# Performance work log

Measured on AMD Instinct MI355X. Metric: run time of the kernel, lower is better.

Reference implementation:

```python
import jax, jax.numpy as jnp
import numpy as np

EPS_LN = 1e-5
EPS_SUM = 1e-5


def setup_inputs() -> dict:
    key = jax.random.key(0)
    ks = jax.random.split(key, 6)
    B, T, F, D = 8, 1024, 512, 64
    x = jax.random.normal(ks[0], (B, T, F), dtype=jnp.float32)
    state = jnp.zeros((B, 1, D * D), dtype=jnp.float32)
    s = 1.0 / np.sqrt(F)
    Wk = jax.random.uniform(ks[1], (F, D), jnp.float32, -s, s)
    Wq = jax.random.uniform(ks[2], (F, D), jnp.float32, -s, s)
    Wv = jax.random.uniform(ks[3], (F, D), jnp.float32, -s, s)
    gamma = jnp.ones((F,), jnp.float32)
    beta = jnp.zeros((F,), jnp.float32)
    return {"x": x, "state": state, "Wk": Wk, "Wq": Wq, "Wv": Wv,
            "gamma": gamma, "beta": beta}


def _layernorm(x, gamma, beta):
    mu = jnp.mean(x, axis=-1, keepdims=True)
    var = jnp.mean(jnp.square(x - mu), axis=-1, keepdims=True)
    return (x - mu) * jax.lax.rsqrt(var + EPS_LN) * gamma + beta


def reference(x, state, Wk, Wq, Wv, gamma, beta):
    B, T, F = x.shape
    D = Wk.shape[1]
    xn = _layernorm(x, gamma, beta)
    K = jax.nn.relu(xn @ Wk)            # [B,T,D]
    Q = jax.nn.relu(xn @ Wq)
    V = xn @ Wv
    # sum normalization (paper)
    K = K / (EPS_SUM + jnp.sum(K, axis=-1, keepdims=True))
    Q = Q / (EPS_SUM + jnp.sum(Q, axis=-1, keepdims=True))
    # outer-product fast weights per step: kv[b,t,i,j] = V[b,t,i] * K[b,t,j]
    kv = jnp.einsum('bti,btj->btij', V, K)        # [B,T,D,D]
    # 'sum' aggregator: running (cumulative) sum seeded by the initial state
    state_seq = state.reshape(B, 1, D, D) + jnp.cumsum(kv, axis=1)  # [B,T,D,D]
    y = jnp.einsum('btij,bti->btj', state_seq, Q)  # [B,T,D]
    return (y, state_seq)
```

## Files before the change

### kernel.cpp

```cpp
#include <hip/hip_runtime.h>

#define BB 8
#define TT 1024
#define FF 512
#define DD 64
#define LCH 16
#define CCH (TT / LCH)
#define PR 8

__device__ __forceinline__ float wave_sum64(float v) {
  #pragma unroll
  for (int m = 32; m >= 1; m >>= 1) v += __shfl_xor(v, m, 64);
  return v;
}

__global__ __launch_bounds__(256, 4) void lnproj_k(
    const float* __restrict__ x,
    const float* __restrict__ gamma, const float* __restrict__ beta,
    const float* __restrict__ Wk, const float* __restrict__ Wq,
    const float* __restrict__ Wv,
    float* __restrict__ Ko, float* __restrict__ Qo, float* __restrict__ Vo) {
  __shared__ float lx[PR * FF];
  __shared__ float part[4 * PR * 3 * DD];
  const int tid = threadIdx.x;
  const int wv = tid >> 6, lane = tid & 63;
  const size_t row0 = (size_t)blockIdx.x * PR;

  {
    const float4* xg = (const float4*)(x + row0 * FF);
    float4* lx4 = (float4*)lx;
    #pragma unroll
    for (int i = 0; i < (PR * FF / 4) / 256; ++i)
      lx4[tid + 256 * i] = xg[tid + 256 * i];
  }
  __syncthreads();

  {
    float g[FF / 64], bt[FF / 64];
    #pragma unroll
    for (int k = 0; k < FF / 64; ++k) {
      g[k]  = gamma[lane + 64 * k];
      bt[k] = beta[lane + 64 * k];
    }
    #pragma unroll
    for (int rr = 0; rr < PR / 4; ++rr) {
      int r = wv * (PR / 4) + rr;
      float v[FF / 64];
      float s = 0.f, ss = 0.f;
      #pragma unroll
      for (int k = 0; k < FF / 64; ++k) {
        v[k] = lx[r * FF + lane + 64 * k];
        s += v[k]; ss += v[k] * v[k];
      }
      s = wave_sum64(s); ss = wave_sum64(ss);
      float m = s * (1.f / FF);
      float var = ss * (1.f / FF) - m * m;
      float rs = rsqrtf(var + 1e-5f);
      #pragma unroll
      for (int k = 0; k < FF / 64; ++k)
        lx[r * FF + lane + 64 * k] = (v[k] - m) * rs * g[k] + bt[k];
    }
  }
  __syncthreads();

  float acc[PR][3];
  #pragma unroll
  for (int r = 0; r < PR; ++r)
    #pragma unroll
    for (int p = 0; p < 3; ++p) acc[r][p] = 0.f;

  const int fbase = wv * (FF / 4);
  #pragma unroll 2
  for (int f0 = fbase; f0 < fbase + FF / 4; f0 += 4) {
    float wk0 = Wk[(f0 + 0) * DD + lane], wk1 = Wk[(f0 + 1) * DD + lane];
    float wk2 = Wk[(f0 + 2) * DD + lane], wk3 = Wk[(f0 + 3) * DD + lane];
    float wq0 = Wq[(f0 + 0) * DD + lane], wq1 = Wq[(f0 + 1) * DD + lane];
    float wq2 = Wq[(f0 + 2) * DD + lane], wq3 = Wq[(f0 + 3) * DD + lane];
    float wv0 = Wv[(f0 + 0) * DD + lane], wv1 = Wv[(f0 + 1) * DD + lane];
    float wv2 = Wv[(f0 + 2) * DD + lane], wv3 = Wv[(f0 + 3) * DD + lane];
    #pragma unroll
    for (int r = 0; r < PR; ++r) {
      float4 xv = *(const float4*)&lx[r * FF + f0];
      acc[r][0] += (xv.x * wk0 + xv.y * wk1) + (xv.z * wk2 + xv.w * wk3);
      acc[r][1] += (xv.x * wq0 + xv.y * wq1) + (xv.z * wq2 + xv.w * wq3);
      acc[r][2] += (xv.x * wv0 + xv.y * wv1) + (xv.z * wv2 + xv.w * wv3);
    }
  }

  #pragma unroll
  for (int r = 0; r < PR; ++r)
    #pragma unroll
    for (int p = 0; p < 3; ++p)
      part[((wv * PR + r) * 3 + p) * DD + lane] = acc[r][p];
  __syncthreads();

  #pragma unroll
  for (int i = 0; i < (PR * 3) / 4; ++i) {
    int pid = wv * ((PR * 3) / 4) + i;
    int r = pid / 3, p = pid - r * 3;
    float val = part[((0 * PR + r) * 3 + p) * DD + lane]
              + part[((1 * PR + r) * 3 + p) * DD + lane]
              + part[((2 * PR + r) * 3 + p) * DD + lane]
              + part[((3 * PR + r) * 3 + p) * DD + lane];
    float* outp = (p == 0) ? Ko : (p == 1) ? Qo : Vo;
    if (p < 2) {
      val = fmaxf(val, 0.f);
      float sm = wave_sum64(val);
      val = val / (1e-5f + sm);
    }
    outp[(row0 + r) * DD + lane] = val;
  }
}

__global__ __launch_bounds__(256) void chunksum_k(const float* __restrict__ Kx,
                                                  const float* __restrict__ Vx,
                                                  float* __restrict__ S) {
  int bc = blockIdx.x, tid = threadIdx.x;
  __shared__ float lk[LCH * DD], lv[LCH * DD];
  for (int e = tid; e < LCH * DD; e += 256) {
    lk[e] = Kx[(size_t)bc * LCH * DD + e];
    lv[e] = Vx[(size_t)bc * LCH * DD + e];
  }
  __syncthreads();
  int j = tid & 63, i0 = (tid >> 6) << 4;
  float acc[16];
  #pragma unroll
  for (int ii = 0; ii < 16; ++ii) acc[ii] = 0.f;
  for (int t = 0; t < LCH; ++t) {
    float kj = lk[t * DD + j];
    #pragma unroll
    for (int ii = 0; ii < 16; ++ii) acc[ii] += lv[t * DD + i0 + ii] * kj;
  }
  float* Sp = S + (size_t)bc * (DD * DD);
  #pragma unroll
  for (int ii = 0; ii < 16; ++ii) Sp[(i0 + ii) * DD + j] = acc[ii];
}

__global__ __launch_bounds__(256) void prefix_k(const float* __restrict__ S,
                                                const float* __restrict__ st0,
                                                float* __restrict__ P) {
  int b = blockIdx.x >> 4;
  int e = ((blockIdx.x & 15) << 8) + threadIdx.x;
  float run = st0[(size_t)b * (DD * DD) + e];
  const float* Sb = S + ((size_t)b * CCH) * (DD * DD) + e;
  float* Pb = P + ((size_t)b * CCH) * (DD * DD) + e;
  for (int c = 0; c < CCH; ++c) {
    Pb[(size_t)c * (DD * DD)] = run;
    run += Sb[(size_t)c * (DD * DD)];
  }
}

__global__ __launch_bounds__(256) void scan_k(const float* __restrict__ Kx,
                     const float* __restrict__ Qx, const float* __restrict__ Vx,
                     const float* __restrict__ P,
                     float* __restrict__ y, float* __restrict__ sout) {
  int bc = blockIdx.x, tid = threadIdx.x;
  int wv = tid >> 6, j = tid & 63;
  int i0 = wv * 16;
  __shared__ float yp[4][LCH][DD];
  float S[16];
  const float* Pp = P + (size_t)bc * (DD * DD);
  #pragma unroll
  for (int ii = 0; ii < 16; ++ii) S[ii] = Pp[(i0 + ii) * DD + j];
  const float* Kb = Kx + (size_t)bc * LCH * DD;
  const float* Vb = Vx + (size_t)bc * LCH * DD;
  const float* Qb = Qx + (size_t)bc * LCH * DD;
  float kreg[LCH];
  #pragma unroll
  for (int t = 0; t < LCH; ++t) kreg[t] = Kb[t * DD + j];
  float* so = sout + (size_t)bc * LCH * (DD * DD) + (size_t)i0 * DD + j;
  for (int t = 0; t < LCH; ++t) {
    const float* Vt = Vb + t * DD + i0;
    const float* Qt = Qb + t * DD + i0;
    float kj = kreg[t];
    float y0 = 0.f, y1 = 0.f, y2 = 0.f, y3 = 0.f;
    float* sot = so + (size_t)t * (DD * DD);
    #pragma unroll
    for (int ii = 0; ii < 16; ii += 4) {
      S[ii]     += Vt[ii]     * kj; sot[(ii)     * DD] = S[ii];     y0 += S[ii]     * Qt[ii];
      S[ii + 1] += Vt[ii + 1] * kj; sot[(ii + 1) * DD] = S[ii + 1]; y1 += S[ii + 1] * Qt[ii + 1];
      S[ii + 2] += Vt[ii + 2] * kj; sot[(ii + 2) * DD] = S[ii + 2]; y2 += S[ii + 2] * Qt[ii + 2];
      S[ii + 3] += Vt[ii + 3] * kj; sot[(ii + 3) * DD] = S[ii + 3]; y3 += S[ii + 3] * Qt[ii + 3];
    }
    yp[wv][t][j] = (y0 + y1) + (y2 + y3);
  }
  __syncthreads();
  float* yo = y + (size_t)bc * LCH * DD;
  #pragma unroll
  for (int tt = 0; tt < LCH / 4; ++tt) {
    int t = wv * (LCH / 4) + tt;
    yo[t * DD + j] = (yp[0][t][j] + yp[1][t][j]) + (yp[2][t][j] + yp[3][t][j]);
  }
}

extern "C" void kernel_launch(void* const* d_in, const int* in_sizes, int n_in,
                              void* d_out, int out_size, void* d_ws, size_t ws_size,
                              hipStream_t stream) {
  const float* x     = (const float*)d_in[0];
  const float* st0   = (const float*)d_in[1];
  const float* Wk    = (const float*)d_in[2];
  const float* Wq    = (const float*)d_in[3];
  const float* Wv    = (const float*)d_in[4];
  const float* gamma = (const float*)d_in[5];
  const float* beta  = (const float*)d_in[6];

  float* out  = (float*)d_out;
  float* yout = out;
  float* sseq = out + (size_t)BB * TT * DD;

  float* ws = (float*)d_ws;
  float* Ko = ws;
  float* Qo = Ko + (size_t)BB * TT * DD;
  float* Vo = Qo + (size_t)BB * TT * DD;
  float* S  = Vo + (size_t)BB * TT * DD;
  float* P  = S  + (size_t)BB * CCH * DD * DD;

  lnproj_k  <<<BB * TT / PR, 256, 0, stream>>>(x, gamma, beta, Wk, Wq, Wv, Ko, Qo, Vo);
  chunksum_k<<<BB * CCH, 256, 0, stream>>>(Ko, Vo, S);
  prefix_k  <<<BB * 16, 256, 0, stream>>>(S, st0, P);
  scan_k    <<<BB * CCH, 256, 0, stream>>>(Ko, Qo, Vo, P, yout, sseq);
}
```

Baseline: 210.3 us.

## Split chunk prefix into parallel segment-sum and segmented-scan kernels

Replaces the serial per-batch prefix over all chunks with a two-pass scheme: first sum chunk states within segments of 8, then each segment scans locally, seeded by the sum of earlier segments. This raises the block count eightfold to expose more parallelism and memory-level concurrency instead of a long dependent loop. It costs an extra kernel launch, an extra read of the chunk-state buffer and a small workspace for segment sums.

```diff
diff --git a/kernel.cpp b/kernel.cpp
--- a/kernel.cpp
+++ b/kernel.cpp
@@ -7,6 +7,8 @@
 #define LCH 16
 #define CCH (TT / LCH)
 #define PR 8
+#define SEG 8
+#define NSEG (CCH / SEG)
 
 __device__ __forceinline__ float wave_sum64(float v) {
   #pragma unroll
@@ -136,17 +138,46 @@
   for (int ii = 0; ii < 16; ++ii) Sp[(i0 + ii) * DD + j] = acc[ii];
 }
 
-__global__ __launch_bounds__(256) void prefix_k(const float* __restrict__ S,
-                                                const float* __restrict__ st0,
-                                                float* __restrict__ P) {
-  int b = blockIdx.x >> 4;
-  int e = ((blockIdx.x & 15) << 8) + threadIdx.x;
+__global__ __launch_bounds__(256) void segsum_k(const float* __restrict__ S,
+                                                float* __restrict__ Z) {
+  int blk = blockIdx.x;
+  int b = blk >> 7;
+  int seg = (blk >> 4) & 7;
+  int e = ((blk & 15) << 8) + threadIdx.x;
+  const float* Sb = S + ((size_t)(b * CCH + seg * SEG)) * (DD * DD) + e;
+  float sv[SEG];
+  #pragma unroll
+  for (int c = 0; c < SEG; ++c) sv[c] = Sb[(size_t)c * (DD * DD)];
+  float acc = 0.f;
+  #pragma unroll
+  for (int c = 0; c < SEG; ++c) acc += sv[c];
+  Z[((size_t)(b * NSEG + seg)) * (DD * DD) + e] = acc;
+}
+
+__global__ __launch_bounds__(256) void segscan_k(const float* __restrict__ S,
+                                                 const float* __restrict__ Z,
+                                                 const float* __restrict__ st0,
+                                                 float* __restrict__ P) {
+  int blk = blockIdx.x;
+  int b = blk >> 7;
+  int seg = (blk >> 4) & 7;
+  int e = ((blk & 15) << 8) + threadIdx.x;
   float run = st0[(size_t)b * (DD * DD) + e];
-  const float* Sb = S + ((size_t)b * CCH) * (DD * DD) + e;
-  float* Pb = P + ((size_t)b * CCH) * (DD * DD) + e;
-  for (int c = 0; c < CCH; ++c) {
+  const float* Zb = Z + (size_t)b * NSEG * (DD * DD) + e;
+  float zv[NSEG - 1];
+  #pragma unroll
+  for (int s = 0; s < NSEG - 1; ++s) zv[s] = Zb[(size_t)s * (DD * DD)];
+  #pragma unroll
+  for (int s = 0; s < NSEG - 1; ++s) if (s < seg) run += zv[s];
+  const float* Sb = S + ((size_t)(b * CCH + seg * SEG)) * (DD * DD) + e;
+  float* Pb = P + ((size_t)(b * CCH + seg * SEG)) * (DD * DD) + e;
+  float sv[SEG];
+  #pragma unroll
+  for (int c = 0; c < SEG; ++c) sv[c] = Sb[(size_t)c * (DD * DD)];
+  #pragma unroll
+  for (int c = 0; c < SEG; ++c) {
     Pb[(size_t)c * (DD * DD)] = run;
-    run += Sb[(size_t)c * (DD * DD)];
+    run += sv[c];
   }
 }
 
@@ -214,9 +245,11 @@
   float* Vo = Qo + (size_t)BB * TT * DD;
   float* S  = Vo + (size_t)BB * TT * DD;
   float* P  = S  + (size_t)BB * CCH * DD * DD;
+  float* Z  = P  + (size_t)BB * CCH * DD * DD;
 
   lnproj_k  <<<BB * TT / PR, 256, 0, stream>>>(x, gamma, beta, Wk, Wq, Wv, Ko, Qo, Vo);
   chunksum_k<<<BB * CCH, 256, 0, stream>>>(Ko, Vo, S);
-  prefix_k  <<<BB * 16, 256, 0, stream>>>(S, st0, P);
+  segsum_k  <<<BB * NSEG * 16, 256, 0, stream>>>(S, Z);
+  segscan_k <<<BB * NSEG * 16, 256, 0, stream>>>(S, Z, st0, P);
   scan_k    <<<BB * CCH, 256, 0, stream>>>(Ko, Qo, Vo, P, yout, sseq);
 }
```

New measurement: 210.5 us. Within noise of the previous version (+0.1%).

## Fuse chunk-sum into projection kernel and parallelize prefix over segments

Applied to the files above, without the earlier changes.

The layernorm/projection kernel now processes a full 16-row chunk per block and computes the chunk's K^T V outer-product sum directly from shared memory, removing a separate kernel and its reload of K and V. The serial 64-step prefix over chunk states is replaced by a segmented version with eight times more blocks: each block re-sums all earlier chunks, then emits prefixes for its own 8 chunks. This trades redundant reads of chunk sums for shorter dependent-load chains and more parallelism. The larger projection tile raises shared memory and register use and halves the block count, which may lower occupancy.

```diff
diff --git a/kernel.cpp b/kernel.cpp
--- a/kernel.cpp
+++ b/kernel.cpp
@@ -6,7 +6,9 @@
 #define DD 64
 #define LCH 16
 #define CCH (TT / LCH)
-#define PR 8
+#define SEG 8
+#define NSEG (CCH / SEG)
+#define EE (DD * DD)
 
 __device__ __forceinline__ float wave_sum64(float v) {
   #pragma unroll
@@ -14,23 +16,25 @@
   return v;
 }
 
-__global__ __launch_bounds__(256, 4) void lnproj_k(
+__global__ __launch_bounds__(256) void lnprojcs_k(
     const float* __restrict__ x,
     const float* __restrict__ gamma, const float* __restrict__ beta,
     const float* __restrict__ Wk, const float* __restrict__ Wq,
     const float* __restrict__ Wv,
-    float* __restrict__ Ko, float* __restrict__ Qo, float* __restrict__ Vo) {
-  __shared__ float lx[PR * FF];
-  __shared__ float part[4 * PR * 3 * DD];
+    float* __restrict__ Ko, float* __restrict__ Qo, float* __restrict__ Vo,
+    float* __restrict__ S) {
+  __shared__ float lx[LCH * FF];
+  __shared__ float part[4 * LCH * 3 * DD];
   const int tid = threadIdx.x;
   const int wv = tid >> 6, lane = tid & 63;
-  const size_t row0 = (size_t)blockIdx.x * PR;
+  const int bc = blockIdx.x;
+  const size_t row0 = (size_t)bc * LCH;
 
   {
     const float4* xg = (const float4*)(x + row0 * FF);
     float4* lx4 = (float4*)lx;
     #pragma unroll
-    for (int i = 0; i < (PR * FF / 4) / 256; ++i)
+    for (int i = 0; i < (LCH * FF / 4) / 256; ++i)
       lx4[tid + 256 * i] = xg[tid + 256 * i];
   }
   __syncthreads();
@@ -43,8 +47,8 @@
       bt[k] = beta[lane + 64 * k];
     }
     #pragma unroll
-    for (int rr = 0; rr < PR / 4; ++rr) {
-      int r = wv * (PR / 4) + rr;
+    for (int rr = 0; rr < LCH / 4; ++rr) {
+      int r = wv * (LCH / 4) + rr;
       float v[FF / 64];
       float s = 0.f, ss = 0.f;
       #pragma unroll
@@ -63,9 +67,9 @@
   }
   __syncthreads();
 
-  float acc[PR][3];
-  #pragma unroll
-  for (int r = 0; r < PR; ++r)
+  float acc[LCH][3];
+  #pragma unroll
+  for (int r = 0; r < LCH; ++r)
     #pragma unroll
     for (int p = 0; p < 3; ++p) acc[r][p] = 0.f;
 
@@ -79,7 +83,7 @@
     float wv0 = Wv[(f0 + 0) * DD + lane], wv1 = Wv[(f0 + 1) * DD + lane];
     float wv2 = Wv[(f0 + 2) * DD + lane], wv3 = Wv[(f0 + 3) * DD + lane];
     #pragma unroll
-    for (int r = 0; r < PR; ++r) {
+    for (int r = 0; r < LCH; ++r) {
       float4 xv = *(const float4*)&lx[r * FF + f0];
       acc[r][0] += (xv.x * wk0 + xv.y * wk1) + (xv.z * wk2 + xv.w * wk3);
       acc[r][1] += (xv.x * wq0 + xv.y * wq1) + (xv.z * wq2 + xv.w * wq3);
@@ -88,65 +92,77 @@
   }
 
   #pragma unroll
-  for (int r = 0; r < PR; ++r)
+  for (int r = 0; r < LCH; ++r)
     #pragma unroll
     for (int p = 0; p < 3; ++p)
-      part[((wv * PR + r) * 3 + p) * DD + lane] = acc[r][p];
-  __syncthreads();
-
-  #pragma unroll
-  for (int i = 0; i < (PR * 3) / 4; ++i) {
-    int pid = wv * ((PR * 3) / 4) + i;
+      part[((wv * LCH + r) * 3 + p) * DD + lane] = acc[r][p];
+  __syncthreads();
+
+  float* lk = lx;
+  float* lv = lx + LCH * DD;
+  #pragma unroll
+  for (int i = 0; i < 12; ++i) {
+    int pid = wv * 12 + i;
     int r = pid / 3, p = pid - r * 3;
-    float val = part[((0 * PR + r) * 3 + p) * DD + lane]
-              + part[((1 * PR + r) * 3 + p) * DD + lane]
-              + part[((2 * PR + r) * 3 + p) * DD + lane]
-              + part[((3 * PR + r) * 3 + p) * DD + lane];
-    float* outp = (p == 0) ? Ko : (p == 1) ? Qo : Vo;
+    float val = part[((0 * LCH + r) * 3 + p) * DD + lane]
+              + part[((1 * LCH + r) * 3 + p) * DD + lane]
+              + part[((2 * LCH + r) * 3 + p) * DD + lane]
+              + part[((3 * LCH + r) * 3 + p) * DD + lane];
     if (p < 2) {
       val = fmaxf(val, 0.f);
       float sm = wave_sum64(val);
       val = val / (1e-5f + sm);
     }
+    float* outp = (p == 0) ? Ko : (p == 1) ? Qo : Vo;
     outp[(row0 + r) * DD + lane] = val;
-  }
-}
-
-__global__ __launch_bounds__(256) void chunksum_k(const float* __restrict__ Kx,
-                                                  const float* __restrict__ Vx,
-                                                  float* __restrict__ S) {
-  int bc = blockIdx.x, tid = threadIdx.x;
-  __shared__ float lk[LCH * DD], lv[LCH * DD];
-  for (int e = tid; e < LCH * DD; e += 256) {
-    lk[e] = Kx[(size_t)bc * LCH * DD + e];
-    lv[e] = Vx[(size_t)bc * LCH * DD + e];
-  }
-  __syncthreads();
-  int j = tid & 63, i0 = (tid >> 6) << 4;
-  float acc[16];
-  #pragma unroll
-  for (int ii = 0; ii < 16; ++ii) acc[ii] = 0.f;
-  for (int t = 0; t < LCH; ++t) {
-    float kj = lk[t * DD + j];
-    #pragma unroll
-    for (int ii = 0; ii < 16; ++ii) acc[ii] += lv[t * DD + i0 + ii] * kj;
-  }
-  float* Sp = S + (size_t)bc * (DD * DD);
-  #pragma unroll
-  for (int ii = 0; ii < 16; ++ii) Sp[(i0 + ii) * DD + j] = acc[ii];
-}
-
-__global__ __launch_bounds__(256) void prefix_k(const float* __restrict__ S,
-                                                const float* __restrict__ st0,
-                                                float* __restrict__ P) {
-  int b = blockIdx.x >> 4;
-  int e = ((blockIdx.x & 15) << 8) + threadIdx.x;
-  float run = st0[(size_t)b * (DD * DD) + e];
-  const float* Sb = S + ((size_t)b * CCH) * (DD * DD) + e;
-  float* Pb = P + ((size_t)b * CCH) * (DD * DD) + e;
-  for (int c = 0; c < CCH; ++c) {
-    Pb[(size_t)c * (DD * DD)] = run;
-    run += Sb[(size_t)c * (DD * DD)];
+    if (p == 0) lk[r * DD + lane] = val;
+    else if (p == 2) lv[r * DD + lane] = val;
+  }
+  __syncthreads();
+
+  {
+    int j = lane, i0 = wv << 4;
+    float a2[16];
+    #pragma unroll
+    for (int ii = 0; ii < 16; ++ii) a2[ii] = 0.f;
+    for (int t = 0; t < LCH; ++t) {
+      float kj = lk[t * DD + j];
+      #pragma unroll
+      for (int ii = 0; ii < 16; ++ii) a2[ii] += lv[t * DD + i0 + ii] * kj;
+    }
+    float* Sp = S + (size_t)bc * EE;
+    #pragma unroll
+    for (int ii = 0; ii < 16; ++ii) Sp[(i0 + ii) * DD + j] = a2[ii];
+  }
+}
+
+__global__ __launch_bounds__(256) void allprefix_k(const float* __restrict__ S,
+                                                   const float* __restrict__ st0,
+                                                   float* __restrict__ P) {
+  int blk = blockIdx.x;
+  int b = blk >> 7;
+  int seg = (blk >> 4) & 7;
+  int e = ((blk & 15) << 8) + threadIdx.x;
+  const float* Sb = S + (size_t)b * CCH * EE + e;
+  float run = st0[(size_t)b * EE + e];
+  const int nprev = seg * SEG;
+  float r0 = 0.f, r1 = 0.f, r2 = 0.f, r3 = 0.f;
+  for (int c = 0; c < nprev; c += 4) {
+    r0 += Sb[(size_t)(c + 0) * EE];
+    r1 += Sb[(size_t)(c + 1) * EE];
+    r2 += Sb[(size_t)(c + 2) * EE];
+    r3 += Sb[(size_t)(c + 3) * EE];
+  }
+  run += (r0 + r1) + (r2 + r3);
+  const float* Ss = Sb + (size_t)nprev * EE;
+  float sv[SEG];
+  #pragma unroll
+  for (int c = 0; c < SEG; ++c) sv[c] = Ss[(size_t)c * EE];
+  float* Pb = P + ((size_t)b * CCH + nprev) * EE + e;
+  #pragma unroll
+  for (int c = 0; c < SEG; ++c) {
+    Pb[(size_t)c * EE] = run;
+    run += sv[c];
   }
 }
 
@@ -159,7 +175,7 @@
   int i0 = wv * 16;
   __shared__ float yp[4][LCH][DD];
   float S[16];
-  const float* Pp = P + (size_t)bc * (DD * DD);
+  const float* Pp = P + (size_t)bc * EE;
   #pragma unroll
   for (int ii = 0; ii < 16; ++ii) S[ii] = Pp[(i0 + ii) * DD + j];
   const float* Kb = Kx + (size_t)bc * LCH * DD;
@@ -168,13 +184,13 @@
   float kreg[LCH];
   #pragma unroll
   for (int t = 0; t < LCH; ++t) kreg[t] = Kb[t * DD + j];
-  float* so = sout + (size_t)bc * LCH * (DD * DD) + (size_t)i0 * DD + j;
+  float* so = sout + (size_t)bc * LCH * EE + (size_t)i0 * DD + j;
   for (int t = 0; t < LCH; ++t) {
     const float* Vt = Vb + t * DD + i0;
     const float* Qt = Qb + t * DD + i0;
     float kj = kreg[t];
     float y0 = 0.f, y1 = 0.f, y2 = 0.f, y3 = 0.f;
-    float* sot = so + (size_t)t * (DD * DD);
+    float* sot = so + (size_t)t * EE;
     #pragma unroll
     for (int ii = 0; ii < 16; ii += 4) {
       S[ii]     += Vt[ii]     * kj; sot[(ii)     * DD] = S[ii];     y0 += S[ii]     * Qt[ii];
@@ -213,10 +229,9 @@
   float* Qo = Ko + (size_t)BB * TT * DD;
   float* Vo = Qo + (size_t)BB * TT * DD;
   float* S  = Vo + (size_t)BB * TT * DD;
-  float* P  = S  + (size_t)BB * CCH * DD * DD;
-
-  lnproj_k  <<<BB * TT / PR, 256, 0, stream>>>(x, gamma, beta, Wk, Wq, Wv, Ko, Qo, Vo);
-  chunksum_k<<<BB * CCH, 256, 0, stream>>>(Ko, Vo, S);
-  prefix_k  <<<BB * 16, 256, 0, stream>>>(S, st0, P);
+  float* P  = S  + (size_t)BB * CCH * EE;
+
+  lnprojcs_k<<<BB * CCH, 256, 0, stream>>>(x, gamma, beta, Wk, Wq, Wv, Ko, Qo, Vo, S);
+  allprefix_k<<<BB * NSEG * 16, 256, 0, stream>>>(S, st0, P);
   scan_k    <<<BB * CCH, 256, 0, stream>>>(Ko, Qo, Vo, P, yout, sseq);
 }
```

New measurement: 212.3 us. No clear change (+0.9%).
